# Kernel optimization log

Hardware: AMD Instinct MI355X
Metric: run time of the kernel (lower is better)

## Reference

```python
import jax, jax.numpy as jnp
import numpy as np

N, E, D_IN, HID, D_OUT, HEADS = 4096, 262144, 256, 256, 128, 4


def gcn_conv(x, edge_index, edge_weight, W, b):
    # PyG GCNConv: linear -> gcn_norm (add self loops, sym norm) -> scatter-add -> +bias
    n = x.shape[0]
    row, col = edge_index[0], edge_index[1]
    loop = jnp.arange(n)
    row_f = jnp.concatenate([row, loop])
    col_f = jnp.concatenate([col, loop])
    ew_f = jnp.concatenate([edge_weight, jnp.ones((n,), edge_weight.dtype)])
    deg = jax.ops.segment_sum(ew_f, col_f, num_segments=n)
    dinv = jnp.where(deg > 0, jax.lax.rsqrt(deg), 0.0)
    norm = dinv[row_f] * ew_f * dinv[col_f]  # [E+N]
    h = x @ W                                # [N, out]
    out = jax.ops.segment_sum(norm[:, None] * h[row_f], col_f, num_segments=n)
    return out + b


def mha(x, in_proj_w, in_proj_b, out_proj_w, out_proj_b):
    # torch.nn.MultiheadAttention, unbatched input [L, Emb], q=k=v=x
    L, Emb = x.shape
    dh = Emb // HEADS
    qkv = x @ in_proj_w.T + in_proj_b
    q, k, v = jnp.split(qkv, 3, axis=-1)
    rs = lambda t: t.reshape(L, HEADS, dh).transpose(1, 0, 2)  # [H, L, dh]
    q, k, v = rs(q), rs(k), rs(v)
    scores = jnp.einsum('hld,hmd->hlm', q, k) / np.float32(np.sqrt(dh))
    attn = jax.nn.softmax(scores, axis=-1)
    o = jnp.einsum('hlm,hmd->hld', attn, v).transpose(1, 0, 2).reshape(L, Emb)
    return o @ out_proj_w.T + out_proj_b


def setup_inputs() -> dict:
    key = jax.random.key(0)
    ks = jax.random.split(key, 12)
    s = 0.02
    return {
        'node_features': jax.random.normal(ks[0], (N, D_IN), jnp.float32),
        'edge_index': jax.random.randint(ks[1], (2, E), 0, N),
        'edge_weight': jax.random.uniform(ks[2], (E,), jnp.float32),
        'W1': jax.random.normal(ks[3], (D_IN, HID), jnp.float32) * s,
        'b1': jnp.zeros((HID,), jnp.float32),
        'W2': jax.random.normal(ks[4], (HID, HID), jnp.float32) * s,
        'b2': jnp.zeros((HID,), jnp.float32),
        'W3': jax.random.normal(ks[5], (HID, D_OUT), jnp.float32) * s,
        'b3': jnp.zeros((D_OUT,), jnp.float32),
        'in_proj_w': jax.random.normal(ks[6], (3 * HID, HID), jnp.float32) * s,
        'in_proj_b': jnp.zeros((3 * HID,), jnp.float32),
        'out_proj_w': jax.random.normal(ks[7], (HID, HID), jnp.float32) * s,
        'out_proj_b': jnp.zeros((HID,), jnp.float32),
    }


def reference(node_features, edge_index, edge_weight, W1, b1, W2, b2, W3, b3,
              in_proj_w, in_proj_b, out_proj_w, out_proj_b):
    ew = edge_weight.astype(jnp.float32)
    x = gcn_conv(node_features, edge_index, ew, W1, b1)
    x = jax.nn.relu(mha(x, in_proj_w, in_proj_b, out_proj_w, out_proj_b))
    # dropout is identity at inference
    x = gcn_conv(x, edge_index, ew, W2, b2)
    x = jax.nn.relu(mha(x, in_proj_w, in_proj_b, out_proj_w, out_proj_b))
    x = gcn_conv(x, edge_index, ew, W3, b3)
    return jax.nn.sigmoid(x)
```

## Files before the change

### kernel.cpp

```cpp
#include <hip/hip_runtime.h>
#include <math.h>

#define N_NODES 4096
#define N_EDGES 262144

typedef __attribute__((ext_vector_type(4))) float f32x4;
typedef __attribute__((ext_vector_type(8))) short s16x8;
typedef __attribute__((ext_vector_type(4))) unsigned short u16x4;

__device__ inline unsigned short f2bf(float f) {
    unsigned u = __builtin_bit_cast(unsigned, f);
    u += 0x7FFF + ((u >> 16) & 1);
    return (unsigned short)(u >> 16);
}
__device__ inline float bf2f(unsigned short u) {
    unsigned x = ((unsigned)u) << 16;
    return __builtin_bit_cast(float, x);
}

#define SWZ(row, colb) (((row) << 7) + ((colb) ^ (((row) & 7) << 4)))

__global__ void init_deg_cnt(float* deg, int* cnt) {
    int i = blockIdx.x * blockDim.x + threadIdx.x;
    if (i < N_NODES) { deg[i] = 1.0f; cnt[i] = 0; }
}

__global__ void deg_accum(const int* __restrict__ col, const float* __restrict__ ew,
                          float* deg, int* cnt) {
    for (int e = blockIdx.x * blockDim.x + threadIdx.x; e < N_EDGES;
         e += gridDim.x * blockDim.x) {
        int c = col[e];
        atomicAdd(&deg[c], ew[e]);
        atomicAdd(&cnt[c], 1);
    }
}

__global__ void finalize_dinv(float* deg) {
    int i = blockIdx.x * blockDim.x + threadIdx.x;
    if (i < N_NODES) { float d = deg[i]; deg[i] = d > 0.f ? rsqrtf(d) : 0.f; }
}

__global__ __launch_bounds__(1024) void scan_offsets(const int* __restrict__ cnt,
                                                     int* off, int* fill) {
    __shared__ int s[1024];
    int tid = threadIdx.x;
    int c0 = cnt[tid * 4 + 0], c1 = cnt[tid * 4 + 1];
    int c2 = cnt[tid * 4 + 2], c3 = cnt[tid * 4 + 3];
    int lsum = c0 + c1 + c2 + c3;
    s[tid] = lsum;
    __syncthreads();
    for (int d = 1; d < 1024; d <<= 1) {
        int v = (tid >= d) ? s[tid - d] : 0;
        __syncthreads();
        s[tid] += v;
        __syncthreads();
    }
    int incl = s[tid];
    int base = incl - lsum;
    int o0 = base, o1 = base + c0, o2 = base + c0 + c1, o3 = base + c0 + c1 + c2;
    off[tid * 4 + 0] = o0;  fill[tid * 4 + 0] = o0;
    off[tid * 4 + 1] = o1;  fill[tid * 4 + 1] = o1;
    off[tid * 4 + 2] = o2;  fill[tid * 4 + 2] = o2;
    off[tid * 4 + 3] = o3;  fill[tid * 4 + 3] = o3;
    if (tid == 1023) off[4096] = incl;
}

__global__ void scatter_edges(const int* __restrict__ row, const int* __restrict__ col,
                              const float* __restrict__ ew, const float* __restrict__ dinv,
                              int* fill, int* srow, float* snorm) {
    for (int e = blockIdx.x * blockDim.x + threadIdx.x; e < N_EDGES;
         e += gridDim.x * blockDim.x) {
        int r = row[e], c = col[e];
        int p = atomicAdd(&fill[c], 1);
        srow[p] = r;
        snorm[p] = dinv[r] * ew[e] * dinv[c];
    }
}

__global__ void conv_bf16(const float* __restrict__ s, unsigned short* __restrict__ d, int n) {
    int i = (blockIdx.x * 256 + threadIdx.x) * 4;
    if (i < n) {
        f32x4 v = *(const f32x4*)(s + i);
        u16x4 o;
#pragma unroll
        for (int j = 0; j < 4; j++) o[j] = f2bf(v[j]);
        *(u16x4*)(d + i) = o;
    }
}

__global__ void conv_ipw(const float* __restrict__ s, unsigned short* __restrict__ d) {
    int i = (blockIdx.x * 256 + threadIdx.x) * 4;
    int r = i >> 8;
    float sc = (r >= 256 && r < 512) ? 0.1803369f : 1.0f;
    f32x4 v = *(const f32x4*)(s + i);
    u16x4 o;
#pragma unroll
    for (int j = 0; j < 4; j++) o[j] = f2bf(v[j] * sc);
    *(u16x4*)(d + i) = o;
}

__global__ void scale_ipb(const float* __restrict__ s, float* __restrict__ d) {
    int i = threadIdx.x;
    float sc = (i >= 256 && i < 512) ? 0.1803369f : 1.0f;
    d[i] = s[i] * sc;
}

__global__ __launch_bounds__(256) void transpose_w(const float* __restrict__ s,
                                                   unsigned short* __restrict__ d, int P) {
    __shared__ float t[32][33];
    int tx = threadIdx.x, ty = threadIdx.y;
    int r0 = blockIdx.y * 32, c0 = blockIdx.x * 32;
#pragma unroll
    for (int q = 0; q < 4; q++)
        t[ty + q * 8][tx] = s[(size_t)(r0 + ty + q * 8) * P + c0 + tx];
    __syncthreads();
#pragma unroll
    for (int q = 0; q < 4; q++)
        d[(size_t)(c0 + ty + q * 8) * 256 + r0 + tx] = f2bf(t[tx][ty + q * 8]);
}

template <bool BIAS, int ACT>
__global__ __launch_bounds__(64) void gemm_bf16(const unsigned short* __restrict__ A,
                                                const unsigned short* __restrict__ B,
                                                const float* __restrict__ bias,
                                                unsigned short* __restrict__ C, int P) {
    int lane = threadIdx.x & 63;
    int lx = lane & 15, g = lane >> 4;
    int brow = blockIdx.y * 16, bcol = blockIdx.x * 64;
    const unsigned short* Ap = A + (size_t)(brow + lx) * 256 + g * 8;
    const unsigned short* Bp = B + (size_t)(bcol + lx) * 256 + g * 8;
    f32x4 acc[4];
#pragma unroll
    for (int nt = 0; nt < 4; nt++) acc[nt] = f32x4{0.f, 0.f, 0.f, 0.f};
#pragma unroll
    for (int kc = 0; kc < 8; kc++) {
        s16x8 a = *(const s16x8*)(Ap + kc * 32);
#pragma unroll
        for (int nt = 0; nt < 4; nt++) {
            s16x8 b = *(const s16x8*)(Bp + (size_t)nt * 16 * 256 + kc * 32);
            acc[nt] = __builtin_amdgcn_mfma_f32_16x16x32_bf16(a, b, acc[nt], 0, 0, 0);
        }
    }
#pragma unroll
    for (int nt = 0; nt < 4; nt++)
#pragma unroll
        for (int r = 0; r < 4; r++) {
            int row = brow + g * 4 + r, col = bcol + nt * 16 + lx;
            float v = acc[nt][r];
            if (BIAS) v += bias[col];
            if (ACT == 1) v = fmaxf(v, 0.f);
            C[(size_t)row * P + col] = f2bf(v);
        }
}

template <int P, bool SIG>
__global__ void gcn_agg(const unsigned short* __restrict__ H, const int* __restrict__ off,
                        const int* __restrict__ srow, const float* __restrict__ snorm,
                        const float* __restrict__ dinv, const float* __restrict__ bias,
                        unsigned short* __restrict__ outb, float* __restrict__ outf) {
    __shared__ int sr[P];
    __shared__ float sw[P];
    int i = blockIdx.x, tid = threadIdx.x;
    float di = dinv[i];
    float acc = di * di * bf2f(H[(size_t)i * P + tid]);
    int beg = off[i], end = off[i + 1];
    for (int base = beg; base < end; base += P) {
        int n = min(P, end - base);
        __syncthreads();
        if (tid < n) { sr[tid] = srow[base + tid]; sw[tid] = snorm[base + tid]; }
        __syncthreads();
#pragma unroll 4
        for (int j = 0; j < n; j++) acc += sw[j] * bf2f(H[(size_t)sr[j] * P + tid]);
    }
    float v = acc + bias[tid];
    if (SIG) {
        v = 1.f / (1.f + exp2f(-v * 1.442695f));
        outf[(size_t)i * P + tid] = v;
    } else {
        outb[(size_t)i * P + tid] = f2bf(v);
    }
}

__global__ __launch_bounds__(256) void prep_v(const unsigned short* __restrict__ qkv,
                                              unsigned short* __restrict__ Vt) {
    __shared__ unsigned short vt[64][66];
    int head = blockIdx.y, n0 = blockIdx.x * 64, tid = threadIdx.x;
#pragma unroll
    for (int it = 0; it < 16; ++it) {
        int idx = tid + it * 256;
        int r = idx >> 6, c = idx & 63;
        vt[c][r] = qkv[(size_t)(n0 + r) * 768 + 512 + head * 64 + c];
    }
    __syncthreads();
#pragma unroll
    for (int it = 0; it < 16; ++it) {
        int idx = tid + it * 256;
        int d = idx >> 6, c = idx & 63;
        Vt[(size_t)(head * 64 + d) * 4096 + n0 + c] = vt[d][c];
    }
}

__global__ __launch_bounds__(256) void attn_mfma(const unsigned short* __restrict__ qkv,
                                                 const unsigned short* __restrict__ Vt,
                                                 unsigned short* __restrict__ Po,
                                                 float* __restrict__ Pl) {
    __shared__ unsigned short Ks[2][64 * 64];
    __shared__ unsigned short Vs[2][64 * 64];
    __shared__ unsigned short Ps[4][16 * 64];

    int tid = threadIdx.x;
    int wid = tid >> 6, lane = tid & 63, g = lane >> 4, lx = lane & 15;
    int head = blockIdx.y, chunk = blockIdx.z;
    int qw = blockIdx.x * 64 + wid * 16;

    s16x8 qa[2];
#pragma unroll
    for (int kc = 0; kc < 2; kc++)
        qa[kc] = *(const s16x8*)(qkv + (size_t)(qw + lx) * 768 + head * 64 + kc * 32 + g * 8);

    const unsigned short* Kg = qkv + 256 + head * 64;
    const unsigned short* VtH = Vt + (size_t)head * 64 * 4096;

    int kr0 = tid >> 3, dc0 = tid & 7;
    int kr1 = kr0 + 32;
    s16x8 stK[2], stV[2];
    auto issue = [&](int kt) {
        stK[0] = *(const s16x8*)(Kg + (size_t)(kt * 64 + kr0) * 768 + dc0 * 8);
        stK[1] = *(const s16x8*)(Kg + (size_t)(kt * 64 + kr1) * 768 + dc0 * 8);
        stV[0] = *(const s16x8*)(VtH + (size_t)kr0 * 4096 + kt * 64 + dc0 * 8);
        stV[1] = *(const s16x8*)(VtH + (size_t)kr1 * 4096 + kt * 64 + dc0 * 8);
    };
    auto commit = [&](int b) {
        *(s16x8*)((char*)Ks[b] + SWZ(kr0, dc0 * 16)) = stK[0];
        *(s16x8*)((char*)Ks[b] + SWZ(kr1, dc0 * 16)) = stK[1];
        *(s16x8*)((char*)Vs[b] + SWZ(kr0, dc0 * 16)) = stV[0];
        *(s16x8*)((char*)Vs[b] + SWZ(kr1, dc0 * 16)) = stV[1];
    };

    float lreg[4] = {0.f, 0.f, 0.f, 0.f};
    f32x4 o[4];
#pragma unroll
    for (int dt = 0; dt < 4; dt++) o[dt] = f32x4{0.f, 0.f, 0.f, 0.f};

    char* PsW = (char*)Ps[wid];

    int kt_beg = chunk * 16, kt_end = kt_beg + 16;
    issue(kt_beg);
    commit(0);
    __syncthreads();

    for (int kt = kt_beg; kt < kt_end; kt++) {
        int cur = (kt - kt_beg) & 1;
        if (kt + 1 < kt_end) issue(kt + 1);

        f32x4 s4[4];
        __builtin_amdgcn_s_setprio(1);
#pragma unroll
        for (int nt = 0; nt < 4; nt++) {
            f32x4 acc = f32x4{0.f, 0.f, 0.f, 0.f};
#pragma unroll
            for (int kc = 0; kc < 2; kc++) {
                s16x8 kb = *(const s16x8*)((char*)Ks[cur] + SWZ(nt * 16 + lx, kc * 64 + g * 16));
                acc = __builtin_amdgcn_mfma_f32_16x16x32_bf16(qa[kc], kb, acc, 0, 0, 0);
            }
            s4[nt] = acc;
        }
        __builtin_amdgcn_s_setprio(0);

#pragma unroll
        for (int nt = 0; nt < 4; nt++)
#pragma unroll
            for (int r = 0; r < 4; r++) {
                float p = exp2f(fminf(s4[nt][r], 60.f));
                lreg[r] += p;
                *(unsigned short*)(PsW + SWZ(4 * g + r, (nt * 16 + lx) * 2)) = f2bf(p);
            }

        __builtin_amdgcn_s_setprio(1);
#pragma unroll
        for (int kc = 0; kc < 2; kc++) {
            s16x8 pa = *(const s16x8*)(PsW + SWZ(lx, kc * 64 + g * 16));
#pragma unroll
            for (int dt = 0; dt < 4; dt++) {
                s16x8 vb = *(const s16x8*)((char*)Vs[cur] + SWZ(dt * 16 + lx, kc * 64 + g * 16));
                o[dt] = __builtin_amdgcn_mfma_f32_16x16x32_bf16(pa, vb, o[dt], 0, 0, 0);
            }
        }
        __builtin_amdgcn_s_setprio(0);

        if (kt + 1 < kt_end) commit(1 - cur);
        __syncthreads();
    }

#pragma unroll
    for (int r = 0; r < 4; r++) {
        float ls = lreg[r];
        ls += __shfl_xor(ls, 1, 16);
        ls += __shfl_xor(ls, 2, 16);
        ls += __shfl_xor(ls, 4, 16);
        ls += __shfl_xor(ls, 8, 16);
        int qrow = qw + 4 * g + r;
        size_t base = (size_t)(chunk * 4 + head) * 4096 + qrow;
        if (lx == 0) Pl[base] = ls;
#pragma unroll
        for (int dt = 0; dt < 4; dt++)
            Po[base * 64 + dt * 16 + lx] = f2bf(o[dt][r]);
    }
}

__global__ __launch_bounds__(256) void attn_combine(const unsigned short* __restrict__ Po,
                                                    const float* __restrict__ Pl,
                                                    unsigned short* __restrict__ att) {
    int q = blockIdx.x;
    int head = threadIdx.x >> 6, d = threadIdx.x & 63;
    float L = 0.f, ov = 0.f;
#pragma unroll
    for (int c = 0; c < 4; c++) {
        size_t base = (size_t)(c * 4 + head) * 4096 + q;
        L += Pl[base];
        ov += bf2f(Po[base * 64 + d]);
    }
    att[(size_t)q * 256 + head * 64 + d] = f2bf(ov / L);
}

extern "C" void kernel_launch(void* const* d_in, const int* in_sizes, int n_in,
                              void* d_out, int out_size, void* d_ws, size_t ws_size,
                              hipStream_t stream) {
    const float* x0  = (const float*)d_in[0];
    const int*   eix = (const int*)d_in[1];
    const float* ew  = (const float*)d_in[2];
    const float* W1  = (const float*)d_in[3];
    const float* b1  = (const float*)d_in[4];
    const float* W2  = (const float*)d_in[5];
    const float* b2  = (const float*)d_in[6];
    const float* W3  = (const float*)d_in[7];
    const float* b3  = (const float*)d_in[8];
    const float* ipw = (const float*)d_in[9];
    const float* ipb = (const float*)d_in[10];
    const float* opw = (const float*)d_in[11];
    const float* opb = (const float*)d_in[12];
    float* out = (float*)d_out;

    char* ws = (char*)d_ws;
    size_t o = 0;
    auto alloc = [&](size_t bytes) -> void* {
        void* p = ws + o;
        o = (o + bytes + 255) & ~size_t(255);
        return p;
    };
    float* dinv  = (float*)alloc(N_NODES * 4);
    int*   cnt   = (int*)alloc(N_NODES * 4);
    int*   off   = (int*)alloc((N_NODES + 1) * 4);
    int*   fill  = (int*)alloc(N_NODES * 4);
    int*   srow  = (int*)alloc(N_EDGES * 4);
    float* snorm = (float*)alloc(N_EDGES * 4);
    unsigned short* x0b  = (unsigned short*)alloc((size_t)N_NODES * 256 * 2);
    unsigned short* W1t  = (unsigned short*)alloc(256 * 256 * 2);
    unsigned short* W2t  = (unsigned short*)alloc(256 * 256 * 2);
    unsigned short* W3t  = (unsigned short*)alloc(128 * 256 * 2);
    unsigned short* ipwb = (unsigned short*)alloc(768 * 256 * 2);
    unsigned short* opwb = (unsigned short*)alloc(256 * 256 * 2);
    float* ipbs          = (float*)alloc(768 * 4);
    unsigned short* Hb   = (unsigned short*)alloc((size_t)N_NODES * 256 * 2);
    unsigned short* XAb  = (unsigned short*)alloc((size_t)N_NODES * 256 * 2);
    unsigned short* XBb  = (unsigned short*)alloc((size_t)N_NODES * 256 * 2);
    unsigned short* QKVb = (unsigned short*)alloc((size_t)N_NODES * 768 * 2);
    unsigned short* Vt   = (unsigned short*)alloc((size_t)4 * 64 * 4096 * 2);
    unsigned short* Po   = (unsigned short*)alloc((size_t)16 * 4096 * 64 * 2);
    float* Pl            = (float*)alloc((size_t)16 * 4096 * 4);

    const int* row = eix;
    const int* col = eix + N_EDGES;

    conv_bf16<<<1024, 256, 0, stream>>>(x0, x0b, N_NODES * 256);
    conv_ipw<<<192, 256, 0, stream>>>(ipw, ipwb);
    conv_bf16<<<64, 256, 0, stream>>>(opw, opwb, 256 * 256);
    scale_ipb<<<1, 768, 0, stream>>>(ipb, ipbs);
    transpose_w<<<dim3(8, 8), dim3(32, 8), 0, stream>>>(W1, W1t, 256);
    transpose_w<<<dim3(8, 8), dim3(32, 8), 0, stream>>>(W2, W2t, 256);
    transpose_w<<<dim3(4, 8), dim3(32, 8), 0, stream>>>(W3, W3t, 128);

    init_deg_cnt<<<16, 256, 0, stream>>>(dinv, cnt);
    deg_accum<<<512, 256, 0, stream>>>(col, ew, dinv, cnt);
    finalize_dinv<<<16, 256, 0, stream>>>(dinv);
    scan_offsets<<<1, 1024, 0, stream>>>(cnt, off, fill);
    scatter_edges<<<512, 256, 0, stream>>>(row, col, ew, dinv, fill, srow, snorm);

    gemm_bf16<false, 0><<<dim3(4, 256), 64, 0, stream>>>(x0b, W1t, nullptr, Hb, 256);
    gcn_agg<256, false><<<N_NODES, 256, 0, stream>>>(Hb, off, srow, snorm, dinv, b1, XAb, nullptr);
    gemm_bf16<true, 0><<<dim3(12, 256), 64, 0, stream>>>(XAb, ipwb, ipbs, QKVb, 768);
    prep_v<<<dim3(64, 4), 256, 0, stream>>>(QKVb, Vt);
    attn_mfma<<<dim3(64, 4, 4), 256, 0, stream>>>(QKVb, Vt, Po, Pl);
    attn_combine<<<N_NODES, 256, 0, stream>>>(Po, Pl, Hb);
    gemm_bf16<true, 1><<<dim3(4, 256), 64, 0, stream>>>(Hb, opwb, opb, XBb, 256);
    gemm_bf16<false, 0><<<dim3(4, 256), 64, 0, stream>>>(XBb, W2t, nullptr, Hb, 256);
    gcn_agg<256, false><<<N_NODES, 256, 0, stream>>>(Hb, off, srow, snorm, dinv, b2, XAb, nullptr);
    gemm_bf16<true, 0><<<dim3(12, 256), 64, 0, stream>>>(XAb, ipwb, ipbs, QKVb, 768);
    prep_v<<<dim3(64, 4), 256, 0, stream>>>(QKVb, Vt);
    attn_mfma<<<dim3(64, 4, 4), 256, 0, stream>>>(QKVb, Vt, Po, Pl);
    attn_combine<<<N_NODES, 256, 0, stream>>>(Po, Pl, Hb);
    gemm_bf16<true, 1><<<dim3(4, 256), 64, 0, stream>>>(Hb, opwb, opb, XBb, 256);
    gemm_bf16<false, 0><<<dim3(2, 256), 64, 0, stream>>>(XBb, W3t, nullptr, Hb, 128);
    gcn_agg<128, true><<<N_NODES, 128, 0, stream>>>(Hb, off, srow, snorm, dinv, b3, nullptr, out);
}
```

Baseline: 354.9 us.

## Fuse prep kernels, fold V transpose into QKV GEMM, widen GEMM tiles, vectorize aggregation

All weight and input conversions and the degree init are merged into one grid-stride prep kernel, and the dinv finalization is folded into the scan kernel. The QKV GEMM now writes V transposed directly, which removes the separate prep_v kernel. GEMM blocks compute 32 rows instead of 16, and gcn_agg runs 64 threads that each handle 4 or 2 channels with vector loads. Attention uses twice as many key chunks (8 instead of 4), which adds split-K parallelism and more work in the combine step. Together these cut launch count and aim to raise per-thread memory efficiency, but the transposes in the prep kernel are now uncoalesced.

```diff
diff --git a/kernel.cpp b/kernel.cpp
--- a/kernel.cpp
+++ b/kernel.cpp
@@ -20,9 +20,83 @@
 
 #define SWZ(row, colb) (((row) << 7) + ((colb) ^ (((row) & 7) << 4)))
 
-__global__ void init_deg_cnt(float* deg, int* cnt) {
-    int i = blockIdx.x * blockDim.x + threadIdx.x;
-    if (i < N_NODES) { deg[i] = 1.0f; cnt[i] = 0; }
+__global__ void prep_all(const float* __restrict__ x0, const float* __restrict__ ipw,
+                         const float* __restrict__ opw, const float* __restrict__ ipb,
+                         const float* __restrict__ W1, const float* __restrict__ W2,
+                         const float* __restrict__ W3,
+                         unsigned short* __restrict__ x0b, unsigned short* __restrict__ ipwb,
+                         unsigned short* __restrict__ opwb, float* __restrict__ ipbs,
+                         unsigned short* __restrict__ W1t, unsigned short* __restrict__ W2t,
+                         unsigned short* __restrict__ W3t,
+                         float* __restrict__ deg, int* __restrict__ cnt) {
+    const int NA = 262144;
+    const int NB = 49152;
+    const int NC = 16384;
+    const int ND1 = 65536, ND2 = 65536, ND3 = 32768;
+    const int NE = 768, NF = 4096;
+    const int total = NA + NB + NC + ND1 + ND2 + ND3 + NE + NF;
+    for (int idx = blockIdx.x * blockDim.x + threadIdx.x; idx < total;
+         idx += gridDim.x * blockDim.x) {
+        int t = idx;
+        if (t < NA) {
+            int i = t * 4;
+            f32x4 v = *(const f32x4*)(x0 + i);
+            u16x4 o;
+#pragma unroll
+            for (int j = 0; j < 4; j++) o[j] = f2bf(v[j]);
+            *(u16x4*)(x0b + i) = o;
+            continue;
+        }
+        t -= NA;
+        if (t < NB) {
+            int i = t * 4;
+            int r = i >> 8;
+            float sc = (r >= 256 && r < 512) ? 0.1803369f : 1.0f;
+            f32x4 v = *(const f32x4*)(ipw + i);
+            u16x4 o;
+#pragma unroll
+            for (int j = 0; j < 4; j++) o[j] = f2bf(v[j] * sc);
+            *(u16x4*)(ipwb + i) = o;
+            continue;
+        }
+        t -= NB;
+        if (t < NC) {
+            int i = t * 4;
+            f32x4 v = *(const f32x4*)(opw + i);
+            u16x4 o;
+#pragma unroll
+            for (int j = 0; j < 4; j++) o[j] = f2bf(v[j]);
+            *(u16x4*)(opwb + i) = o;
+            continue;
+        }
+        t -= NC;
+        if (t < ND1) {
+            int r = t & 255, c = t >> 8;
+            W1t[c * 256 + r] = f2bf(W1[r * 256 + c]);
+            continue;
+        }
+        t -= ND1;
+        if (t < ND2) {
+            int r = t & 255, c = t >> 8;
+            W2t[c * 256 + r] = f2bf(W2[r * 256 + c]);
+            continue;
+        }
+        t -= ND2;
+        if (t < ND3) {
+            int r = t & 255, c = t >> 8;
+            W3t[c * 256 + r] = f2bf(W3[r * 128 + c]);
+            continue;
+        }
+        t -= ND3;
+        if (t < NE) {
+            float sc = (t >= 256 && t < 512) ? 0.1803369f : 1.0f;
+            ipbs[t] = ipb[t] * sc;
+            continue;
+        }
+        t -= NE;
+        deg[t] = 1.0f;
+        cnt[t] = 0;
+    }
 }
 
 __global__ void deg_accum(const int* __restrict__ col, const float* __restrict__ ew,
@@ -35,15 +109,17 @@
     }
 }
 
-__global__ void finalize_dinv(float* deg) {
-    int i = blockIdx.x * blockDim.x + threadIdx.x;
-    if (i < N_NODES) { float d = deg[i]; deg[i] = d > 0.f ? rsqrtf(d) : 0.f; }
-}
-
 __global__ __launch_bounds__(1024) void scan_offsets(const int* __restrict__ cnt,
+                                                     float* __restrict__ deg,
                                                      int* off, int* fill) {
     __shared__ int s[1024];
     int tid = threadIdx.x;
+#pragma unroll
+    for (int q = 0; q < 4; q++) {
+        int i = tid * 4 + q;
+        float d = deg[i];
+        deg[i] = d > 0.f ? rsqrtf(d) : 0.f;
+    }
     int c0 = cnt[tid * 4 + 0], c1 = cnt[tid * 4 + 1];
     int c2 = cnt[tid * 4 + 2], c3 = cnt[tid * 4 + 3];
     int lsum = c0 + c1 + c2 + c3;
@@ -77,126 +153,124 @@
     }
 }
 
-__global__ void conv_bf16(const float* __restrict__ s, unsigned short* __restrict__ d, int n) {
-    int i = (blockIdx.x * 256 + threadIdx.x) * 4;
-    if (i < n) {
-        f32x4 v = *(const f32x4*)(s + i);
-        u16x4 o;
-#pragma unroll
-        for (int j = 0; j < 4; j++) o[j] = f2bf(v[j]);
-        *(u16x4*)(d + i) = o;
-    }
-}
-
-__global__ void conv_ipw(const float* __restrict__ s, unsigned short* __restrict__ d) {
-    int i = (blockIdx.x * 256 + threadIdx.x) * 4;
-    int r = i >> 8;
-    float sc = (r >= 256 && r < 512) ? 0.1803369f : 1.0f;
-    f32x4 v = *(const f32x4*)(s + i);
-    u16x4 o;
-#pragma unroll
-    for (int j = 0; j < 4; j++) o[j] = f2bf(v[j] * sc);
-    *(u16x4*)(d + i) = o;
-}
-
-__global__ void scale_ipb(const float* __restrict__ s, float* __restrict__ d) {
-    int i = threadIdx.x;
-    float sc = (i >= 256 && i < 512) ? 0.1803369f : 1.0f;
-    d[i] = s[i] * sc;
-}
-
-__global__ __launch_bounds__(256) void transpose_w(const float* __restrict__ s,
-                                                   unsigned short* __restrict__ d, int P) {
-    __shared__ float t[32][33];
-    int tx = threadIdx.x, ty = threadIdx.y;
-    int r0 = blockIdx.y * 32, c0 = blockIdx.x * 32;
-#pragma unroll
-    for (int q = 0; q < 4; q++)
-        t[ty + q * 8][tx] = s[(size_t)(r0 + ty + q * 8) * P + c0 + tx];
-    __syncthreads();
-#pragma unroll
-    for (int q = 0; q < 4; q++)
-        d[(size_t)(c0 + ty + q * 8) * 256 + r0 + tx] = f2bf(t[tx][ty + q * 8]);
-}
-
-template <bool BIAS, int ACT>
+template <bool BIAS, int ACT, bool QKV>
 __global__ __launch_bounds__(64) void gemm_bf16(const unsigned short* __restrict__ A,
                                                 const unsigned short* __restrict__ B,
                                                 const float* __restrict__ bias,
-                                                unsigned short* __restrict__ C, int P) {
+                                                unsigned short* __restrict__ C,
+                                                unsigned short* __restrict__ Vt, int P) {
     int lane = threadIdx.x & 63;
     int lx = lane & 15, g = lane >> 4;
-    int brow = blockIdx.y * 16, bcol = blockIdx.x * 64;
-    const unsigned short* Ap = A + (size_t)(brow + lx) * 256 + g * 8;
+    int brow = blockIdx.y * 32, bcol = blockIdx.x * 64;
+    const unsigned short* Ap0 = A + (size_t)(brow + lx) * 256 + g * 8;
+    const unsigned short* Ap1 = Ap0 + 16 * 256;
     const unsigned short* Bp = B + (size_t)(bcol + lx) * 256 + g * 8;
-    f32x4 acc[4];
-#pragma unroll
-    for (int nt = 0; nt < 4; nt++) acc[nt] = f32x4{0.f, 0.f, 0.f, 0.f};
+    f32x4 acc[2][4];
+#pragma unroll
+    for (int mi = 0; mi < 2; mi++)
+#pragma unroll
+        for (int nt = 0; nt < 4; nt++) acc[mi][nt] = f32x4{0.f, 0.f, 0.f, 0.f};
 #pragma unroll
     for (int kc = 0; kc < 8; kc++) {
-        s16x8 a = *(const s16x8*)(Ap + kc * 32);
+        s16x8 a0 = *(const s16x8*)(Ap0 + kc * 32);
+        s16x8 a1 = *(const s16x8*)(Ap1 + kc * 32);
 #pragma unroll
         for (int nt = 0; nt < 4; nt++) {
             s16x8 b = *(const s16x8*)(Bp + (size_t)nt * 16 * 256 + kc * 32);
-            acc[nt] = __builtin_amdgcn_mfma_f32_16x16x32_bf16(a, b, acc[nt], 0, 0, 0);
-        }
-    }
-#pragma unroll
-    for (int nt = 0; nt < 4; nt++)
-#pragma unroll
-        for (int r = 0; r < 4; r++) {
-            int row = brow + g * 4 + r, col = bcol + nt * 16 + lx;
-            float v = acc[nt][r];
-            if (BIAS) v += bias[col];
-            if (ACT == 1) v = fmaxf(v, 0.f);
-            C[(size_t)row * P + col] = f2bf(v);
-        }
+            acc[0][nt] = __builtin_amdgcn_mfma_f32_16x16x32_bf16(a0, b, acc[0][nt], 0, 0, 0);
+            acc[1][nt] = __builtin_amdgcn_mfma_f32_16x16x32_bf16(a1, b, acc[1][nt], 0, 0, 0);
+        }
+    }
+    bool isV = QKV && (bcol >= 512);
+    if (!isV) {
+#pragma unroll
+        for (int mi = 0; mi < 2; mi++)
+#pragma unroll
+            for (int nt = 0; nt < 4; nt++)
+#pragma unroll
+                for (int r = 0; r < 4; r++) {
+                    int row = brow + mi * 16 + g * 4 + r, col = bcol + nt * 16 + lx;
+                    float v = acc[mi][nt][r];
+                    if (BIAS) v += bias[col];
+                    if (ACT == 1) v = fmaxf(v, 0.f);
+                    C[(size_t)row * P + col] = f2bf(v);
+                }
+    } else {
+        int head = (bcol - 512) >> 6;
+#pragma unroll
+        for (int mi = 0; mi < 2; mi++)
+#pragma unroll
+            for (int nt = 0; nt < 4; nt++) {
+                int col = bcol + nt * 16 + lx;
+                u16x4 vv;
+#pragma unroll
+                for (int r = 0; r < 4; r++) {
+                    float v = acc[mi][nt][r];
+                    if (BIAS) v += bias[col];
+                    vv[r] = f2bf(v);
+                }
+                *(u16x4*)(Vt + (size_t)(head * 64 + nt * 16 + lx) * 4096 +
+                          brow + mi * 16 + g * 4) = vv;
+            }
+    }
 }
 
 template <int P, bool SIG>
-__global__ void gcn_agg(const unsigned short* __restrict__ H, const int* __restrict__ off,
-                        const int* __restrict__ srow, const float* __restrict__ snorm,
-                        const float* __restrict__ dinv, const float* __restrict__ bias,
-                        unsigned short* __restrict__ outb, float* __restrict__ outf) {
-    __shared__ int sr[P];
-    __shared__ float sw[P];
+__global__ __launch_bounds__(64) void gcn_agg(const unsigned short* __restrict__ H,
+                                              const int* __restrict__ off,
+                                              const int* __restrict__ srow,
+                                              const float* __restrict__ snorm,
+                                              const float* __restrict__ dinv,
+                                              const float* __restrict__ bias,
+                                              unsigned short* __restrict__ outb,
+                                              float* __restrict__ outf) {
+    constexpr int CPT = P / 64;
+    __shared__ int sr[64];
+    __shared__ float sw[64];
     int i = blockIdx.x, tid = threadIdx.x;
     float di = dinv[i];
-    float acc = di * di * bf2f(H[(size_t)i * P + tid]);
+    float d2 = di * di;
+    float acc[CPT];
+    if (CPT == 4) {
+        u16x4 h = *(const u16x4*)(H + (size_t)i * P + tid * 4);
+#pragma unroll
+        for (int j = 0; j < 4; j++) acc[j] = d2 * bf2f(h[j]);
+    } else {
+        unsigned h = *(const unsigned*)(H + (size_t)i * P + tid * 2);
+        acc[0] = d2 * bf2f((unsigned short)(h & 0xFFFF));
+        acc[1] = d2 * bf2f((unsigned short)(h >> 16));
+    }
     int beg = off[i], end = off[i + 1];
-    for (int base = beg; base < end; base += P) {
-        int n = min(P, end - base);
+    for (int base = beg; base < end; base += 64) {
+        int n = min(64, end - base);
         __syncthreads();
         if (tid < n) { sr[tid] = srow[base + tid]; sw[tid] = snorm[base + tid]; }
         __syncthreads();
 #pragma unroll 4
-        for (int j = 0; j < n; j++) acc += sw[j] * bf2f(H[(size_t)sr[j] * P + tid]);
-    }
-    float v = acc + bias[tid];
-    if (SIG) {
-        v = 1.f / (1.f + exp2f(-v * 1.442695f));
-        outf[(size_t)i * P + tid] = v;
-    } else {
-        outb[(size_t)i * P + tid] = f2bf(v);
-    }
-}
-
-__global__ __launch_bounds__(256) void prep_v(const unsigned short* __restrict__ qkv,
-                                              unsigned short* __restrict__ Vt) {
-    __shared__ unsigned short vt[64][66];
-    int head = blockIdx.y, n0 = blockIdx.x * 64, tid = threadIdx.x;
-#pragma unroll
-    for (int it = 0; it < 16; ++it) {
-        int idx = tid + it * 256;
-        int r = idx >> 6, c = idx & 63;
-        vt[c][r] = qkv[(size_t)(n0 + r) * 768 + 512 + head * 64 + c];
-    }
-    __syncthreads();
-#pragma unroll
-    for (int it = 0; it < 16; ++it) {
-        int idx = tid + it * 256;
-        int d = idx >> 6, c = idx & 63;
-        Vt[(size_t)(head * 64 + d) * 4096 + n0 + c] = vt[d][c];
+        for (int j = 0; j < n; j++) {
+            float w = sw[j];
+            size_t rb = (size_t)sr[j] * P;
+            if (CPT == 4) {
+                u16x4 h = *(const u16x4*)(H + rb + tid * 4);
+#pragma unroll
+                for (int q = 0; q < 4; q++) acc[q] += w * bf2f(h[q]);
+            } else {
+                unsigned h = *(const unsigned*)(H + rb + tid * 2);
+                acc[0] += w * bf2f((unsigned short)(h & 0xFFFF));
+                acc[1] += w * bf2f((unsigned short)(h >> 16));
+            }
+        }
+    }
+#pragma unroll
+    for (int j = 0; j < CPT; j++) {
+        int c = tid * CPT + j;
+        float v = acc[j] + bias[c];
+        if (SIG) {
+            v = 1.f / (1.f + exp2f(-v * 1.442695f));
+            outf[(size_t)i * P + c] = v;
+        } else {
+            outb[(size_t)i * P + c] = f2bf(v);
+        }
     }
 }
 
@@ -244,7 +318,7 @@
 
     char* PsW = (char*)Ps[wid];
 
-    int kt_beg = chunk * 16, kt_end = kt_beg + 16;
+    int kt_beg = chunk * 8, kt_end = kt_beg + 8;
     issue(kt_beg);
     commit(0);
     __syncthreads();
@@ -315,7 +389,7 @@
     int head = threadIdx.x >> 6, d = threadIdx.x & 63;
     float L = 0.f, ov = 0.f;
 #pragma unroll
-    for (int c = 0; c < 4; c++) {
+    for (int c = 0; c < 8; c++) {
         size_t base = (size_t)(c * 4 + head) * 4096 + q;
         L += Pl[base];
         ov += bf2f(Po[base * 64 + d]);
@@ -366,40 +440,30 @@
     unsigned short* XBb  = (unsigned short*)alloc((size_t)N_NODES * 256 * 2);
     unsigned short* QKVb = (unsigned short*)alloc((size_t)N_NODES * 768 * 2);
     unsigned short* Vt   = (unsigned short*)alloc((size_t)4 * 64 * 4096 * 2);
-    unsigned short* Po   = (unsigned short*)alloc((size_t)16 * 4096 * 64 * 2);
-    float* Pl            = (float*)alloc((size_t)16 * 4096 * 4);
+    unsigned short* Po   = (unsigned short*)alloc((size_t)32 * 4096 * 64 * 2);
+    float* Pl            = (float*)alloc((size_t)32 * 4096 * 4);
 
     const int* row = eix;
     const int* col = eix + N_EDGES;
 
-    conv_bf16<<<1024, 256, 0, stream>>>(x0, x0b, N_NODES * 256);
-    conv_ipw<<<192, 256, 0, stream>>>(ipw, ipwb);
-    conv_bf16<<<64, 256, 0, stream>>>(opw, opwb, 256 * 256);
-    scale_ipb<<<1, 768, 0, stream>>>(ipb, ipbs);
-    transpose_w<<<dim3(8, 8), dim3(32, 8), 0, stream>>>(W1, W1t, 256);
-    transpose_w<<<dim3(8, 8), dim3(32, 8), 0, stream>>>(W2, W2t, 256);
-    transpose_w<<<dim3(4, 8), dim3(32, 8), 0, stream>>>(W3, W3t, 128);
-
-    init_deg_cnt<<<16, 256, 0, stream>>>(dinv, cnt);
+    prep_all<<<1024, 256, 0, stream>>>(x0, ipw, opw, ipb, W1, W2, W3,
+                                       x0b, ipwb, opwb, ipbs, W1t, W2t, W3t, dinv, cnt);
     deg_accum<<<512, 256, 0, stream>>>(col, ew, dinv, cnt);
-    finalize_dinv<<<16, 256, 0, stream>>>(dinv);
-    scan_offsets<<<1, 1024, 0, stream>>>(cnt, off, fill);
+    scan_offsets<<<1, 1024, 0, stream>>>(cnt, dinv, off, fill);
     scatter_edges<<<512, 256, 0, stream>>>(row, col, ew, dinv, fill, srow, snorm);
 
-    gemm_bf16<false, 0><<<dim3(4, 256), 64, 0, stream>>>(x0b, W1t, nullptr, Hb, 256);
-    gcn_agg<256, false><<<N_NODES, 256, 0, stream>>>(Hb, off, srow, snorm, dinv, b1, XAb, nullptr);
-    gemm_bf16<true, 0><<<dim3(12, 256), 64, 0, stream>>>(XAb, ipwb, ipbs, QKVb, 768);
-    prep_v<<<dim3(64, 4), 256, 0, stream>>>(QKVb, Vt);
-    attn_mfma<<<dim3(64, 4, 4), 256, 0, stream>>>(QKVb, Vt, Po, Pl);
+    gemm_bf16<false, 0, false><<<dim3(4, 128), 64, 0, stream>>>(x0b, W1t, nullptr, Hb, nullptr, 256);
+    gcn_agg<256, false><<<N_NODES, 64, 0, stream>>>(Hb, off, srow, snorm, dinv, b1, XAb, nullptr);
+    gemm_bf16<true, 0, true><<<dim3(12, 128), 64, 0, stream>>>(XAb, ipwb, ipbs, QKVb, Vt, 768);
+    attn_mfma<<<dim3(64, 4, 8), 256, 0, stream>>>(QKVb, Vt, Po, Pl);
     attn_combine<<<N_NODES, 256, 0, stream>>>(Po, Pl, Hb);
-    gemm_bf16<true, 1><<<dim3(4, 256), 64, 0, stream>>>(Hb, opwb, opb, XBb, 256);
-    gemm_bf16<false, 0><<<dim3(4, 256), 64, 0, stream>>>(XBb, W2t, nullptr, Hb, 256);
-    gcn_agg<256, false><<<N_NODES, 256, 0, stream>>>(Hb, off, srow, snorm, dinv, b2, XAb, nullptr);
-    gemm_bf16<true, 0><<<dim3(12, 256), 64, 0, stream>>>(XAb, ipwb, ipbs, QKVb, 768);
-    prep_v<<<dim3(64, 4), 256, 0, stream>>>(QKVb, Vt);
-    attn_mfma<<<dim3(64, 4, 4), 256, 0, stream>>>(QKVb, Vt, Po, Pl);
+    gemm_bf16<true, 1, false><<<dim3(4, 128), 64, 0, stream>>>(Hb, opwb, opb, XBb, nullptr, 256);
+    gemm_bf16<false, 0, false><<<dim3(4, 128), 64, 0, stream>>>(XBb, W2t, nullptr, Hb, nullptr, 256);
+    gcn_agg<256, false><<<N_NODES, 64, 0, stream>>>(Hb, off, srow, snorm, dinv, b2, XAb, nullptr);
+    gemm_bf16<true, 0, true><<<dim3(12, 128), 64, 0, stream>>>(XAb, ipwb, ipbs, QKVb, Vt, 768);
+    attn_mfma<<<dim3(64, 4, 8), 256, 0, stream>>>(QKVb, Vt, Po, Pl);
     attn_combine<<<N_NODES, 256, 0, stream>>>(Po, Pl, Hb);
-    gemm_bf16<true, 1><<<dim3(4, 256), 64, 0, stream>>>(Hb, opwb, opb, XBb, 256);
-    gemm_bf16<false, 0><<<dim3(2, 256), 64, 0, stream>>>(XBb, W3t, nullptr, Hb, 128);
-    gcn_agg<128, true><<<N_NODES, 128, 0, stream>>>(Hb, off, srow, snorm, dinv, b3, nullptr, out);
-}
+    gemm_bf16<true, 1, false><<<dim3(4, 128), 64, 0, stream>>>(Hb, opwb, opb, XBb, nullptr, 256);
+    gemm_bf16<false, 0, false><<<dim3(2, 128), 64, 0, stream>>>(XBb, W3t, nullptr, Hb, nullptr, 128);
+    gcn_agg<128, true><<<N_NODES, 64, 0, stream>>>(Hb, off, srow, snorm, dinv, b3, nullptr, out);
+}
```

Result: faster. 309.7 us (-12.8%).
